# Kernel optimization log

Measured on AMD Instinct MI355X. Metric: run time of the kernel, lower is better.

## Reference

```python
import jax, jax.numpy as jnp
import numpy as np

EPS = 1e-6
WEACH = 10  # width chunk size


def layernorm2d(x, w, b):
    # channel-wise LN per (b,h,w): x [B,C,H,W]
    mu = x.mean(axis=1, keepdims=True)
    var = ((x - mu) ** 2).mean(axis=1, keepdims=True)
    y = (x - mu) / jnp.sqrt(var + EPS)
    return w[None, :, None, None] * y + b[None, :, None, None]


def conv1x1(x, w, b):
    # w [O,I], x [B,I,H,W]
    return jnp.einsum('oi,bihw->bohw', w, x) + b[None, :, None, None]


def dynamic_conv1x1(x, y, fc1w, fc1b, fc2w, fc2b, W, bias):
    # attention2d on y -> per-sample mixture over K expert 1x1 convs applied to x
    gap = y.mean(axis=(2, 3))                          # [B,C]
    a = jax.nn.relu(gap @ fc1w.T + fc1b)               # [B,K]
    a = a @ fc2w.T + fc2b                              # [B,K]
    att = jax.nn.softmax(a, axis=-1)                   # [B,K]
    Wagg = jnp.einsum('bk,koi->boi', att, W)           # [B,O,I]
    bagg = att @ bias                                  # [B,O]
    return jnp.einsum('boi,bihw->bohw', Wagg, x) + bagg[:, :, None, None]


def _chunk(t, nW):
    # [B,C,H,W] -> [B,C,H,nW,WEACH]
    B, C, H, W = t.shape
    return t.reshape(B, C, H, nW, WEACH)


def reference(x_l, x_r,
              norm_l_w, norm_l_b, norm_r_w, norm_r_b,
              lp1_w, lp1_b, rp1_w, rp1_b,
              lp2_w, lp2_b, rp2_w, rp2_b,
              beta, gamma,
              lf_fc1w, lf_fc1b, lf_fc2w, lf_fc2b, lf_W, lf_bias,
              rf_fc1w, rf_fc1b, rf_fc2w, rf_fc2b, rf_W, rf_bias):
    B, C, H, W = x_l.shape
    nW = W // WEACH
    scale = C ** (-0.5)

    # LayerNorm and 1x1 projections are pointwise -> compute on full tensor
    Ql = _chunk(conv1x1(layernorm2d(x_l, norm_l_w, norm_l_b), lp1_w, lp1_b), nW)
    Qr = _chunk(conv1x1(layernorm2d(x_r, norm_r_w, norm_r_b), rp1_w, rp1_b), nW)
    Vl = _chunk(conv1x1(x_l, lp2_w, lp2_b), nW)
    Vr = _chunk(conv1x1(x_r, rp2_w, rp2_b), nW)

    # block-diagonal attention within each width chunk, per height row
    attn = jnp.einsum('bchnu,bchnv->bhnuv', Ql, Qr) * scale   # [B,H,nW,10,10]
    A_r2l = jax.nn.softmax(attn, axis=-1)                     # softmax over v (right positions)
    A_l2r = jax.nn.softmax(attn, axis=-2)                     # softmax over u (left positions)
    F_r2l = jnp.einsum('bhnuv,bchnv->bchnu', A_r2l, Vr)       # [B,C,H,nW,10]
    F_l2r = jnp.einsum('bhnuv,bchnu->bchnv', A_l2r, Vl)

    F_r2l = F_r2l.reshape(B, C, H, W) * beta
    F_l2r = F_l2r.reshape(B, C, H, W) * gamma

    # dynamic per-batch 1x1 grouped conv, conditioned on the shortcut branch
    out_rl = dynamic_conv1x1(F_r2l, x_l, lf_fc1w, lf_fc1b, lf_fc2w, lf_fc2b, lf_W, lf_bias)
    out_lr = dynamic_conv1x1(F_l2r, x_r, rf_fc1w, rf_fc1b, rf_fc2w, rf_fc2b, rf_W, rf_bias)
    return (x_l + out_rl, x_r + out_lr)


def setup_inputs() -> dict:
    C, K = 64, 3
    B, H, W = 4, 180, 320
    key = jax.random.key(0)
    ks = jax.random.split(key, 24)
    n = lambda k, s, sc=0.05: jax.random.normal(k, s, dtype=jnp.float32) * sc
    return {
        'x_l': jax.random.normal(ks[0], (B, C, H, W), dtype=jnp.float32),
        'x_r': jax.random.normal(ks[1], (B, C, H, W), dtype=jnp.float32),
        'norm_l_w': jnp.ones((C,), jnp.float32), 'norm_l_b': jnp.zeros((C,), jnp.float32),
        'norm_r_w': jnp.ones((C,), jnp.float32), 'norm_r_b': jnp.zeros((C,), jnp.float32),
        'lp1_w': n(ks[2], (C, C)), 'lp1_b': jnp.zeros((C,), jnp.float32),
        'rp1_w': n(ks[3], (C, C)), 'rp1_b': jnp.zeros((C,), jnp.float32),
        'lp2_w': n(ks[4], (C, C)), 'lp2_b': jnp.zeros((C,), jnp.float32),
        'rp2_w': n(ks[5], (C, C)), 'rp2_b': jnp.zeros((C,), jnp.float32),
        'beta': n(ks[6], (1, C, 1, 1), 0.1), 'gamma': n(ks[7], (1, C, 1, 1), 0.1),
        'lf_fc1w': n(ks[8], (K, C)), 'lf_fc1b': jnp.zeros((K,), jnp.float32),
        'lf_fc2w': n(ks[9], (K, K)), 'lf_fc2b': jnp.zeros((K,), jnp.float32),
        'lf_W': n(ks[10], (K, C, C)), 'lf_bias': n(ks[11], (K, C), 0.01),
        'rf_fc1w': n(ks[12], (K, C)), 'rf_fc1b': jnp.zeros((K,), jnp.float32),
        'rf_fc2w': n(ks[13], (K, K)), 'rf_fc2b': jnp.zeros((K,), jnp.float32),
        'rf_W': n(ks[14], (K, C, C)), 'rf_bias': n(ks[15], (K, C), 0.01),
    }
```

## Files before the change

### kernel.cpp

```cpp
#include <hip/hip_runtime.h>

typedef unsigned int u32;

#define BB 4
#define HH 180
#define WWD 320
#define HW_ 57600
#define TENSOR_ 14745600
#define XM 84
#define QS 68

__device__ __align__(16) float g_gap[512];
__device__ __align__(16) float g_bagg[512];
__device__ __align__(16) float g_swn[128];
__device__ __align__(16) float g_sb[128];
__device__ __align__(16) float g_waggT[32768];
__device__ __align__(16) float g_w1fT[8192];
__device__ __align__(16) float g_p2T[8192];

__global__ __launch_bounds__(256) void gap_kernel(const float* __restrict__ xl,
                                                  const float* __restrict__ xr) {
    int job = blockIdx.x;
    int side = job >> 8;
    int bc = job & 255;
    const float4* p = (const float4*)((side ? xr : xl) + (size_t)bc * HW_);
    float s = 0.f;
    for (int i = threadIdx.x; i < 14400; i += 256) {
        float4 v = p[i];
        s += v.x + v.y + v.z + v.w;
    }
    #pragma unroll
    for (int off = 32; off > 0; off >>= 1) s += __shfl_down(s, off, 64);
    __shared__ float red[4];
    int lane = threadIdx.x & 63, wv = threadIdx.x >> 6;
    if (lane == 0) red[wv] = s;
    __syncthreads();
    if (threadIdx.x == 0)
        g_gap[job] = (red[0] + red[1] + red[2] + red[3]) * (1.f / 57600.f);
}

__global__ __launch_bounds__(256) void prep_kernel(
    const float* __restrict__ nlw, const float* __restrict__ nlb,
    const float* __restrict__ nrw, const float* __restrict__ nrb,
    const float* __restrict__ lp1w, const float* __restrict__ rp1w,
    const float* __restrict__ lp2w, const float* __restrict__ rp2w,
    const float* __restrict__ lf1w, const float* __restrict__ lf1b,
    const float* __restrict__ lf2w, const float* __restrict__ lf2b,
    const float* __restrict__ lfbias,
    const float* __restrict__ rf1w, const float* __restrict__ rf1b,
    const float* __restrict__ rf2w, const float* __restrict__ rf2b,
    const float* __restrict__ rfbias,
    const float* __restrict__ lfW, const float* __restrict__ rfW)
{
    __shared__ float att[2][4][3];
    int t = threadIdx.x;
    if (t < 8) {
        int side = t >> 2, b = t & 3;
        const float* f1w = side ? rf1w : lf1w;
        const float* f1b = side ? rf1b : lf1b;
        const float* f2w = side ? rf2w : lf2w;
        const float* f2bv = side ? rf2b : lf2b;
        const float* g = g_gap + side*256 + b*64;
        float a1[3];
        #pragma unroll
        for (int k = 0; k < 3; k++) {
            float s = f1b[k];
            for (int c = 0; c < 64; c++) s += g[c] * f1w[k*64 + c];
            a1[k] = fmaxf(s, 0.f);
        }
        float a2[3];
        #pragma unroll
        for (int j = 0; j < 3; j++) {
            float s = f2bv[j];
            #pragma unroll
            for (int k = 0; k < 3; k++) s += a1[k] * f2w[j*3 + k];
            a2[j] = s;
        }
        float m = fmaxf(fmaxf(a2[0], a2[1]), a2[2]);
        float e0 = __expf(a2[0]-m), e1 = __expf(a2[1]-m), e2 = __expf(a2[2]-m);
        float inv = 1.f / (e0 + e1 + e2);
        att[side][b][0] = e0*inv; att[side][b][1] = e1*inv; att[side][b][2] = e2*inv;
    }
    __syncthreads();

    if (blockIdx.x < 16) {
        int flat = blockIdx.x * 2048 + t * 8;
        int side = flat >> 14, bb = (flat >> 12) & 3, i = (flat >> 6) & 63, o0 = flat & 63;
        const float* Wp = side ? rfW : lfW;
        float a0 = att[side][bb][0], a1 = att[side][bb][1], a2 = att[side][bb][2];
        #pragma unroll
        for (int q = 0; q < 8; q++) {
            int o = o0 + q;
            g_waggT[flat+q] = a0*Wp[o*64+i] + a1*Wp[4096+o*64+i] + a2*Wp[8192+o*64+i];
        }
    } else {
        if (t < 128) {
            int side = t >> 6, o = t & 63;
            const float* w1 = side ? rp1w : lp1w;
            const float* w2 = side ? rp2w : lp2w;
            const float* nw = side ? nrw : nlw;
            const float* nb = side ? nrb : nlb;
            float s_wn = 0.f, s_b = 0.f;
            for (int i = 0; i < 64; i++) {
                float wf = w1[o*64 + i];
                float wp = wf * nw[i];
                g_w1fT[side*4096 + i*64 + o] = wp;
                g_p2T [side*4096 + i*64 + o] = w2[o*64 + i];
                s_wn += wp;
                s_b  += wf * nb[i];
            }
            g_swn[side*64 + o] = s_wn;
            g_sb[side*64 + o]  = s_b;
        }
        for (int idx = t; idx < 512; idx += 256) {
            int side = idx >> 8, r = idx & 255, b = r >> 6, o = r & 63;
            const float* bp = side ? rfbias : lfbias;
            g_bagg[idx] = att[side][b][0]*bp[o]
                        + att[side][b][1]*bp[64+o]
                        + att[side][b][2]*bp[128+o];
        }
    }
}

__global__ __launch_bounds__(256, 3) void main_kernel(
    const float* __restrict__ xl_g, const float* __restrict__ xr_g,
    const float* __restrict__ lp1b, const float* __restrict__ rp1b,
    const float* __restrict__ lp2b, const float* __restrict__ rp2b,
    const float* __restrict__ beta, const float* __restrict__ gamma,
    float* __restrict__ out)
{
    __shared__ __align__(16) float xi0[2688];
    __shared__ __align__(16) float xi1[2688];
    __shared__ __align__(16) float qf0[2720];
    __shared__ __align__(16) float qf1[2720];
    __shared__ float attn[4][10][10];
    __shared__ float Ar[4][10][10];
    __shared__ float Al[4][10][10];
    __shared__ float muA[40], rsA[40], muB[40], rsB[40];

    int t = threadIdx.x;
    int wv = t >> 6, lane = t & 63;
    int bid = blockIdx.x;
    int b  = bid / (HH*8);
    int r0 = bid % (HH*8);
    int h  = r0 / 8;
    int g  = r0 % 8;
    int w0 = g * 40;

    for (int idx = t; idx < 640; idx += 256) {
        int tensor = idx / 320;
        int r2 = idx - tensor*320;
        int m = r2 / 10, seg = r2 - m*10;
        const float* src = (tensor ? xr_g : xl_g)
                         + (((size_t)(b*64 + 2*m)*HH + h)*WWD + w0 + seg*4);
        float4 a = *(const float4*)(src);
        float4 c = *(const float4*)(src + HW_);
        float* dst = (tensor ? xi1 : xi0) + m*XM + seg*8;
        *(float4*)(dst)     = make_float4(a.x, c.x, a.y, c.y);
        *(float4*)(dst + 4) = make_float4(a.z, c.z, a.w, c.w);
    }
    __syncthreads();

    if (lane < 20) {
        int side = wv >> 1;
        int u = (wv & 1)*20 + lane;
        const float* xx = side ? xi1 : xi0;
        float s = 0.f, s2 = 0.f;
        for (int m = 0; m < 32; m++) {
            float v0 = xx[m*XM + u*2];
            float v1 = xx[m*XM + u*2 + 1];
            s += v0 + v1; s2 += v0*v0 + v1*v1;
        }
        float mu = s * (1.f/64.f);
        float var = fmaxf(s2 * (1.f/64.f) - mu*mu, 0.f);
        float rs = rsqrtf(var + 1e-6f);
        if (side) { muB[u] = mu; rsB[u] = rs; } else { muA[u] = mu; rsA[u] = rs; }
    }
    __syncthreads();

    int og = lane & 7, ug = lane >> 3;
    int ob = og * 8, ub = ug * 5;

    float acc[8][5];
    #pragma unroll
    for (int r = 0; r < 8; r++)
        #pragma unroll
        for (int j = 0; j < 5; j++) acc[r][j] = 0.f;

    {
        const float* wT; const float* xs;
        switch (wv) {
            case 0:  wT = g_w1fT;        xs = xi0; break;
            case 1:  wT = g_w1fT + 4096; xs = xi1; break;
            case 2:  wT = g_p2T;         xs = xi0; break;
            default: wT = g_p2T + 4096;  xs = xi1; break;
        }
        __builtin_amdgcn_s_setprio(1);
        for (int m = 0; m < 32; m++) {
            const float* wp = wT + m*128;
            float4 wa0 = *(const float4*)(wp + ob);
            float4 wa1 = *(const float4*)(wp + ob + 4);
            float4 wb0 = *(const float4*)(wp + 64 + ob);
            float4 wb1 = *(const float4*)(wp + 64 + ob + 4);
            float2 xv[5];
            const float* xrow = xs + m*XM + ub*2;
            #pragma unroll
            for (int j = 0; j < 5; j++) xv[j] = *(const float2*)(xrow + j*2);
            float wa[8] = {wa0.x,wa0.y,wa0.z,wa0.w, wa1.x,wa1.y,wa1.z,wa1.w};
            float wb[8] = {wb0.x,wb0.y,wb0.z,wb0.w, wb1.x,wb1.y,wb1.z,wb1.w};
            #pragma unroll
            for (int r = 0; r < 8; r++)
                #pragma unroll
                for (int j = 0; j < 5; j++) {
                    acc[r][j] = fmaf(wa[r], xv[j].x, acc[r][j]);
                    acc[r][j] = fmaf(wb[r], xv[j].y, acc[r][j]);
                }
        }
        __builtin_amdgcn_s_setprio(0);
    }

    if (wv < 2) {
        const float* mu  = wv ? muB : muA;
        const float* rs  = wv ? rsB : rsA;
        const float* p1b = wv ? rp1b : lp1b;
        float* qdst = wv ? qf1 : qf0;
        float swl[8], sbl[8];
        #pragma unroll
        for (int r = 0; r < 8; r++) {
            swl[r] = g_swn[wv*64 + ob + r];
            sbl[r] = g_sb[wv*64 + ob + r] + p1b[ob + r];
        }
        #pragma unroll
        for (int j = 0; j < 5; j++) {
            int u = ub + j;
            float rsv = rs[u], muv = mu[u];
            float e[8];
            #pragma unroll
            for (int r = 0; r < 8; r++)
                e[r] = rsv*(acc[r][j] - muv*swl[r]) + sbl[r];
            *(float4*)(qdst + u*QS + ob)     = make_float4(e[0],e[1],e[2],e[3]);
            *(float4*)(qdst + u*QS + ob + 4) = make_float4(e[4],e[5],e[6],e[7]);
        }
    } else {
        const float* p2b = (wv == 2) ? lp2b : rp2b;
        #pragma unroll
        for (int r = 0; r < 8; r++) {
            float bv = p2b[ob + r];
            #pragma unroll
            for (int j = 0; j < 5; j++) acc[r][j] += bv;
        }
    }
    __syncthreads();

    for (int p = lane; p < 100; p += 64) {
        int uu = p / 10, vv = p - (p/10)*10;
        const float4* ra = (const float4*)(qf0 + (wv*10 + uu)*QS);
        const float4* rb = (const float4*)(qf1 + (wv*10 + vv)*QS);
        float s = 0.f;
        #pragma unroll
        for (int cc = 0; cc < 16; cc++) {
            float4 a = ra[cc], q = rb[cc];
            s += a.x*q.x + a.y*q.y + a.z*q.z + a.w*q.w;
        }
        attn[wv][uu][vv] = s * 0.125f;
    }
    __syncthreads();

    if (t < 40) {
        int k = t / 10, uu = t - (t/10)*10;
        float m = attn[k][uu][0];
        #pragma unroll
        for (int v2 = 1; v2 < 10; v2++) m = fmaxf(m, attn[k][uu][v2]);
        float e[10]; float ssum = 0.f;
        #pragma unroll
        for (int v2 = 0; v2 < 10; v2++) { e[v2] = __expf(attn[k][uu][v2] - m); ssum += e[v2]; }
        float inv = 1.f / ssum;
        #pragma unroll
        for (int v2 = 0; v2 < 10; v2++) Ar[k][uu][v2] = e[v2]*inv;
    } else if (t >= 64 && t < 104) {
        int t2 = t - 64;
        int k = t2 / 10, vv = t2 - (t2/10)*10;
        float m = attn[k][0][vv];
        #pragma unroll
        for (int u2 = 1; u2 < 10; u2++) m = fmaxf(m, attn[k][u2][vv]);
        float e[10]; float ssum = 0.f;
        #pragma unroll
        for (int u2 = 0; u2 < 10; u2++) { e[u2] = __expf(attn[k][u2][vv] - m); ssum += e[u2]; }
        float inv = 1.f / ssum;
        #pragma unroll
        for (int u2 = 0; u2 < 10; u2++) Al[k][u2][vv] = e[u2]*inv;
    }
    __syncthreads();

    if (wv == 3) {
        int k = ug >> 1, half = ug & 1, vb = half*5;
        float sc[8];
        #pragma unroll
        for (int r = 0; r < 8; r++) sc[r] = beta[ob + r];
        #pragma unroll
        for (int j2 = 0; j2 < 5; j2++) {
            int u1 = vb + j2;
            int u2 = 5 - vb + j2;
            float a1[5], a2[5];
            #pragma unroll
            for (int j = 0; j < 5; j++) { a1[j] = Ar[k][u1][vb+j]; a2[j] = Ar[k][u2][vb+j]; }
            #pragma unroll
            for (int r = 0; r < 8; r++) {
                float sA = 0.f, sB = 0.f;
                #pragma unroll
                for (int j = 0; j < 5; j++) {
                    sA = fmaf(a1[j], acc[r][j], sA);
                    sB = fmaf(a2[j], acc[r][j], sB);
                }
                float recv = __shfl_xor(sB, 8, 64);
                int o = ob + r;
                qf0[(o>>1)*XM + (k*10 + u1)*2 + (o&1)] = (sA + recv) * sc[r];
            }
        }
    } else if (wv == 2) {
        int k = ug >> 1, half = ug & 1, vb = half*5;
        float sc[8];
        #pragma unroll
        for (int r = 0; r < 8; r++) sc[r] = gamma[ob + r];
        #pragma unroll
        for (int j2 = 0; j2 < 5; j2++) {
            int u1 = vb + j2;
            int u2 = 5 - vb + j2;
            float a1[5], a2[5];
            #pragma unroll
            for (int j = 0; j < 5; j++) { a1[j] = Al[k][vb+j][u1]; a2[j] = Al[k][vb+j][u2]; }
            #pragma unroll
            for (int r = 0; r < 8; r++) {
                float sA = 0.f, sB = 0.f;
                #pragma unroll
                for (int j = 0; j < 5; j++) {
                    sA = fmaf(a1[j], acc[r][j], sA);
                    sB = fmaf(a2[j], acc[r][j], sB);
                }
                float recv = __shfl_xor(sB, 8, 64);
                int o = ob + r;
                qf1[(o>>1)*XM + (k*10 + u1)*2 + (o&1)] = (sA + recv) * sc[r];
            }
        }
    }
    __syncthreads();

    {
        int side = wv >> 1;
        int oh   = wv & 1;
        int ob4  = oh*32 + og*4;
        const float* Fb   = side ? qf1 : qf0;
        const float* xres = side ? xi1 : xi0;
        const float* wrow = g_waggT + (size_t)(side*4 + b)*4096;
        float acc5[4][5];
        #pragma unroll
        for (int r = 0; r < 4; r++)
            #pragma unroll
            for (int j = 0; j < 5; j++) acc5[r][j] = 0.f;
        __builtin_amdgcn_s_setprio(1);
        for (int m = 0; m < 32; m++) {
            const float* wp = wrow + m*128;
            float4 wa4 = *(const float4*)(wp + ob4);
            float4 wb4 = *(const float4*)(wp + 64 + ob4);
            float2 xv[5];
            const float* frow = Fb + m*XM + ub*2;
            #pragma unroll
            for (int j = 0; j < 5; j++) xv[j] = *(const float2*)(frow + j*2);
            float wa[4] = {wa4.x,wa4.y,wa4.z,wa4.w};
            float wb[4] = {wb4.x,wb4.y,wb4.z,wb4.w};
            #pragma unroll
            for (int r = 0; r < 4; r++)
                #pragma unroll
                for (int j = 0; j < 5; j++) {
                    acc5[r][j] = fmaf(wa[r], xv[j].x, acc5[r][j]);
                    acc5[r][j] = fmaf(wb[r], xv[j].y, acc5[r][j]);
                }
        }
        __builtin_amdgcn_s_setprio(0);
        #pragma unroll
        for (int r = 0; r < 4; r++) {
            int o = ob4 + r;
            float bg = g_bagg[side*256 + b*64 + o];
            float* op = out + (size_t)side*TENSOR_ + (((size_t)(b*64+o)*HH + h)*WWD + w0 + ub);
            #pragma unroll
            for (int j = 0; j < 5; j++)
                op[j] = acc5[r][j] + bg + xres[(o>>1)*XM + (ub+j)*2 + (o&1)];
        }
    }
}

extern "C" void kernel_launch(void* const* d_in, const int* in_sizes, int n_in,
                              void* d_out, int out_size, void* d_ws, size_t ws_size,
                              hipStream_t stream) {
    (void)in_sizes; (void)n_in; (void)out_size; (void)d_ws; (void)ws_size;
    const float* x_l = (const float*)d_in[0];
    const float* x_r = (const float*)d_in[1];

    gap_kernel<<<512, 256, 0, stream>>>(x_l, x_r);
    prep_kernel<<<17, 256, 0, stream>>>(
        (const float*)d_in[2],  (const float*)d_in[3],
        (const float*)d_in[4],  (const float*)d_in[5],
        (const float*)d_in[6],  (const float*)d_in[8],
        (const float*)d_in[10], (const float*)d_in[12],
        (const float*)d_in[16], (const float*)d_in[17],
        (const float*)d_in[18], (const float*)d_in[19], (const float*)d_in[21],
        (const float*)d_in[22], (const float*)d_in[23],
        (const float*)d_in[24], (const float*)d_in[25], (const float*)d_in[27],
        (const float*)d_in[20], (const float*)d_in[26]);
    main_kernel<<<BB*HH*8, 256, 0, stream>>>(x_l, x_r,
        (const float*)d_in[7],  (const float*)d_in[9],
        (const float*)d_in[11], (const float*)d_in[13],
        (const float*)d_in[14], (const float*)d_in[15],
        (float*)d_out);
}
```

Measured before the change: 482.1 us.

## Convert LDS tiles and weights to packed fp16 and use fdot2 for projections

Weights, input tiles and intermediate Q/F features are now stored as packed half2 in shared memory and global scratch. The 1x1 projection, attention-score and output conv loops use v_dot2 (fdot2) with fp32 accumulation instead of pairs of fp32 FMAs. Shared memory per block is roughly halved and occupancy hints rise from 3 to 5 blocks. The residual is reloaded from global fp32 instead of the LDS copy. Precision drops to fp16 inputs, which risks accuracy for LayerNorm statistics and the residual path.

Measured after the change: 436.5 us. 9.5% less time.

```diff
diff --git a/kernel.cpp b/kernel.cpp
--- a/kernel.cpp
+++ b/kernel.cpp
@@ -1,22 +1,25 @@
 #include <hip/hip_runtime.h>
 
 typedef unsigned int u32;
+typedef __fp16 h2 __attribute__((ext_vector_type(2)));
 
 #define BB 4
 #define HH 180
 #define WWD 320
 #define HW_ 57600
 #define TENSOR_ 14745600
-#define XM 84
-#define QS 68
+#define XST 44
+#define QST 36
+
+union U4 { float4 f; h2 h[4]; };
 
 __device__ __align__(16) float g_gap[512];
 __device__ __align__(16) float g_bagg[512];
 __device__ __align__(16) float g_swn[128];
 __device__ __align__(16) float g_sb[128];
-__device__ __align__(16) float g_waggT[32768];
-__device__ __align__(16) float g_w1fT[8192];
-__device__ __align__(16) float g_p2T[8192];
+__device__ __align__(16) h2 g_w1fTh[4096];
+__device__ __align__(16) h2 g_p2Th[4096];
+__device__ __align__(16) h2 g_waggTh[16384];
 
 __global__ __launch_bounds__(256) void gap_kernel(const float* __restrict__ xl,
                                                   const float* __restrict__ xr) {
@@ -84,14 +87,16 @@
     __syncthreads();
 
     if (blockIdx.x < 16) {
-        int flat = blockIdx.x * 2048 + t * 8;
-        int side = flat >> 14, bb = (flat >> 12) & 3, i = (flat >> 6) & 63, o0 = flat & 63;
+        int flat2 = blockIdx.x * 1024 + t * 4;
+        int side = flat2 >> 13, bb = (flat2 >> 11) & 3, m = (flat2 >> 6) & 31, o0 = flat2 & 63;
         const float* Wp = side ? rfW : lfW;
         float a0 = att[side][bb][0], a1 = att[side][bb][1], a2 = att[side][bb][2];
         #pragma unroll
-        for (int q = 0; q < 8; q++) {
+        for (int q = 0; q < 4; q++) {
             int o = o0 + q;
-            g_waggT[flat+q] = a0*Wp[o*64+i] + a1*Wp[4096+o*64+i] + a2*Wp[8192+o*64+i];
+            float wi0 = a0*Wp[o*64+2*m]   + a1*Wp[4096+o*64+2*m]   + a2*Wp[8192+o*64+2*m];
+            float wi1 = a0*Wp[o*64+2*m+1] + a1*Wp[4096+o*64+2*m+1] + a2*Wp[8192+o*64+2*m+1];
+            g_waggTh[((side*4+bb)*32 + m)*64 + o] = __builtin_amdgcn_cvt_pkrtz(wi0, wi1);
         }
     } else {
         if (t < 128) {
@@ -101,13 +106,15 @@
             const float* nw = side ? nrw : nlw;
             const float* nb = side ? nrb : nlb;
             float s_wn = 0.f, s_b = 0.f;
-            for (int i = 0; i < 64; i++) {
-                float wf = w1[o*64 + i];
-                float wp = wf * nw[i];
-                g_w1fT[side*4096 + i*64 + o] = wp;
-                g_p2T [side*4096 + i*64 + o] = w2[o*64 + i];
-                s_wn += wp;
-                s_b  += wf * nb[i];
+            for (int m = 0; m < 32; m++) {
+                float wf0 = w1[o*64 + 2*m],   wf1 = w1[o*64 + 2*m+1];
+                float wp0 = wf0 * nw[2*m],    wp1 = wf1 * nw[2*m+1];
+                h2 hw = __builtin_amdgcn_cvt_pkrtz(wp0, wp1);
+                g_w1fTh[side*2048 + m*64 + o] = hw;
+                g_p2Th [side*2048 + m*64 + o] =
+                    __builtin_amdgcn_cvt_pkrtz(w2[o*64+2*m], w2[o*64+2*m+1]);
+                s_wn += (float)hw.x + (float)hw.y;
+                s_b  += wf0*nb[2*m] + wf1*nb[2*m+1];
             }
             g_swn[side*64 + o] = s_wn;
             g_sb[side*64 + o]  = s_b;
@@ -122,17 +129,17 @@
     }
 }
 
-__global__ __launch_bounds__(256, 3) void main_kernel(
+__global__ __launch_bounds__(256, 5) void main_kernel(
     const float* __restrict__ xl_g, const float* __restrict__ xr_g,
     const float* __restrict__ lp1b, const float* __restrict__ rp1b,
     const float* __restrict__ lp2b, const float* __restrict__ rp2b,
     const float* __restrict__ beta, const float* __restrict__ gamma,
     float* __restrict__ out)
 {
-    __shared__ __align__(16) float xi0[2688];
-    __shared__ __align__(16) float xi1[2688];
-    __shared__ __align__(16) float qf0[2720];
-    __shared__ __align__(16) float qf1[2720];
+    __shared__ __align__(16) h2 xi0[1408];
+    __shared__ __align__(16) h2 xi1[1408];
+    __shared__ __align__(16) h2 qf0[1440];
+    __shared__ __align__(16) h2 qf1[1440];
     __shared__ float attn[4][10][10];
     __shared__ float Ar[4][10][10];
     __shared__ float Al[4][10][10];
@@ -155,22 +162,31 @@
                          + (((size_t)(b*64 + 2*m)*HH + h)*WWD + w0 + seg*4);
         float4 a = *(const float4*)(src);
         float4 c = *(const float4*)(src + HW_);
-        float* dst = (tensor ? xi1 : xi0) + m*XM + seg*8;
-        *(float4*)(dst)     = make_float4(a.x, c.x, a.y, c.y);
-        *(float4*)(dst + 4) = make_float4(a.z, c.z, a.w, c.w);
+        U4 u;
+        u.h[0] = __builtin_amdgcn_cvt_pkrtz(a.x, c.x);
+        u.h[1] = __builtin_amdgcn_cvt_pkrtz(a.y, c.y);
+        u.h[2] = __builtin_amdgcn_cvt_pkrtz(a.z, c.z);
+        u.h[3] = __builtin_amdgcn_cvt_pkrtz(a.w, c.w);
+        h2* dst = (tensor ? xi1 : xi0) + m*XST + seg*4;
+        *(float4*)dst = u.f;
     }
     __syncthreads();
 
     if (lane < 20) {
         int side = wv >> 1;
         int u = (wv & 1)*20 + lane;
-        const float* xx = side ? xi1 : xi0;
-        float s = 0.f, s2 = 0.f;
-        for (int m = 0; m < 32; m++) {
-            float v0 = xx[m*XM + u*2];
-            float v1 = xx[m*XM + u*2 + 1];
-            s += v0 + v1; s2 += v0*v0 + v1*v1;
-        }
+        const h2* xx = side ? xi1 : xi0;
+        h2 one2; one2.x = (__fp16)1.f; one2.y = (__fp16)1.f;
+        float s_0 = 0.f, s_1 = 0.f, q_0 = 0.f, q_1 = 0.f;
+        for (int m = 0; m < 32; m += 2) {
+            h2 v0 = xx[m*XST + u];
+            h2 v1 = xx[(m+1)*XST + u];
+            s_0 = __builtin_amdgcn_fdot2(v0, one2, s_0, false);
+            q_0 = __builtin_amdgcn_fdot2(v0, v0,   q_0, false);
+            s_1 = __builtin_amdgcn_fdot2(v1, one2, s_1, false);
+            q_1 = __builtin_amdgcn_fdot2(v1, v1,   q_1, false);
+        }
+        float s = s_0 + s_1, s2 = q_0 + q_1;
         float mu = s * (1.f/64.f);
         float var = fmaxf(s2 * (1.f/64.f) - mu*mu, 0.f);
         float rs = rsqrtf(var + 1e-6f);
@@ -188,33 +204,30 @@
         for (int j = 0; j < 5; j++) acc[r][j] = 0.f;
 
     {
-        const float* wT; const float* xs;
+        const h2* wT; const h2* xs;
         switch (wv) {
-            case 0:  wT = g_w1fT;        xs = xi0; break;
-            case 1:  wT = g_w1fT + 4096; xs = xi1; break;
-            case 2:  wT = g_p2T;         xs = xi0; break;
-            default: wT = g_p2T + 4096;  xs = xi1; break;
+            case 0:  wT = g_w1fTh;        xs = xi0; break;
+            case 1:  wT = g_w1fTh + 2048; xs = xi1; break;
+            case 2:  wT = g_p2Th;         xs = xi0; break;
+            default: wT = g_p2Th + 2048;  xs = xi1; break;
         }
         __builtin_amdgcn_s_setprio(1);
         for (int m = 0; m < 32; m++) {
-            const float* wp = wT + m*128;
-            float4 wa0 = *(const float4*)(wp + ob);
-            float4 wa1 = *(const float4*)(wp + ob + 4);
-            float4 wb0 = *(const float4*)(wp + 64 + ob);
-            float4 wb1 = *(const float4*)(wp + 64 + ob + 4);
-            float2 xv[5];
-            const float* xrow = xs + m*XM + ub*2;
-            #pragma unroll
-            for (int j = 0; j < 5; j++) xv[j] = *(const float2*)(xrow + j*2);
-            float wa[8] = {wa0.x,wa0.y,wa0.z,wa0.w, wa1.x,wa1.y,wa1.z,wa1.w};
-            float wb[8] = {wb0.x,wb0.y,wb0.z,wb0.w, wb1.x,wb1.y,wb1.z,wb1.w};
+            const h2* wp = wT + m*64 + ob;
+            U4 w0u, w1u;
+            w0u.f = *(const float4*)(wp);
+            w1u.f = *(const float4*)(wp + 4);
+            h2 xv[5];
+            const h2* xrow = xs + m*XST + ub;
+            #pragma unroll
+            for (int j = 0; j < 5; j++) xv[j] = xrow[j];
+            h2 wa[8] = {w0u.h[0],w0u.h[1],w0u.h[2],w0u.h[3],
+                        w1u.h[0],w1u.h[1],w1u.h[2],w1u.h[3]};
             #pragma unroll
             for (int r = 0; r < 8; r++)
                 #pragma unroll
-                for (int j = 0; j < 5; j++) {
-                    acc[r][j] = fmaf(wa[r], xv[j].x, acc[r][j]);
-                    acc[r][j] = fmaf(wb[r], xv[j].y, acc[r][j]);
-                }
+                for (int j = 0; j < 5; j++)
+                    acc[r][j] = __builtin_amdgcn_fdot2(wa[r], xv[j], acc[r][j], false);
         }
         __builtin_amdgcn_s_setprio(0);
     }
@@ -223,7 +236,7 @@
         const float* mu  = wv ? muB : muA;
         const float* rs  = wv ? rsB : rsA;
         const float* p1b = wv ? rp1b : lp1b;
-        float* qdst = wv ? qf1 : qf0;
+        h2* qdst = wv ? qf1 : qf0;
         float swl[8], sbl[8];
         #pragma unroll
         for (int r = 0; r < 8; r++) {
@@ -238,8 +251,12 @@
             #pragma unroll
             for (int r = 0; r < 8; r++)
                 e[r] = rsv*(acc[r][j] - muv*swl[r]) + sbl[r];
-            *(float4*)(qdst + u*QS + ob)     = make_float4(e[0],e[1],e[2],e[3]);
-            *(float4*)(qdst + u*QS + ob + 4) = make_float4(e[4],e[5],e[6],e[7]);
+            U4 q;
+            q.h[0] = __builtin_amdgcn_cvt_pkrtz(e[0], e[1]);
+            q.h[1] = __builtin_amdgcn_cvt_pkrtz(e[2], e[3]);
+            q.h[2] = __builtin_amdgcn_cvt_pkrtz(e[4], e[5]);
+            q.h[3] = __builtin_amdgcn_cvt_pkrtz(e[6], e[7]);
+            *(float4*)(qdst + u*QST + og*4) = q.f;
         }
     } else {
         const float* p2b = (wv == 2) ? lp2b : rp2b;
@@ -254,15 +271,17 @@
 
     for (int p = lane; p < 100; p += 64) {
         int uu = p / 10, vv = p - (p/10)*10;
-        const float4* ra = (const float4*)(qf0 + (wv*10 + uu)*QS);
-        const float4* rb = (const float4*)(qf1 + (wv*10 + vv)*QS);
-        float s = 0.f;
-        #pragma unroll
-        for (int cc = 0; cc < 16; cc++) {
-            float4 a = ra[cc], q = rb[cc];
-            s += a.x*q.x + a.y*q.y + a.z*q.z + a.w*q.w;
-        }
-        attn[wv][uu][vv] = s * 0.125f;
+        const h2* ra = qf0 + (wv*10 + uu)*QST;
+        const h2* rb = qf1 + (wv*10 + vv)*QST;
+        float sa = 0.f, sb = 0.f, sc = 0.f, sd = 0.f;
+        #pragma unroll
+        for (int c2 = 0; c2 < 32; c2 += 4) {
+            sa = __builtin_amdgcn_fdot2(ra[c2],   rb[c2],   sa, false);
+            sb = __builtin_amdgcn_fdot2(ra[c2+1], rb[c2+1], sb, false);
+            sc = __builtin_amdgcn_fdot2(ra[c2+2], rb[c2+2], sc, false);
+            sd = __builtin_amdgcn_fdot2(ra[c2+3], rb[c2+3], sd, false);
+        }
+        attn[wv][uu][vv] = ((sa+sb)+(sc+sd)) * 0.125f;
     }
     __syncthreads();
 
@@ -304,6 +323,7 @@
             float a1[5], a2[5];
             #pragma unroll
             for (int j = 0; j < 5; j++) { a1[j] = Ar[k][u1][vb+j]; a2[j] = Ar[k][u2][vb+j]; }
+            float fv[8];
             #pragma unroll
             for (int r = 0; r < 8; r++) {
                 float sA = 0.f, sB = 0.f;
@@ -313,9 +333,12 @@
                     sB = fmaf(a2[j], acc[r][j], sB);
                 }
                 float recv = __shfl_xor(sB, 8, 64);
-                int o = ob + r;
-                qf0[(o>>1)*XM + (k*10 + u1)*2 + (o&1)] = (sA + recv) * sc[r];
+                fv[r] = (sA + recv) * sc[r];
             }
+            #pragma unroll
+            for (int rr = 0; rr < 4; rr++)
+                qf0[(og*4+rr)*XST + k*10 + u1] =
+                    __builtin_amdgcn_cvt_pkrtz(fv[2*rr], fv[2*rr+1]);
         }
     } else if (wv == 2) {
         int k = ug >> 1, half = ug & 1, vb = half*5;
@@ -329,6 +352,7 @@
             float a1[5], a2[5];
             #pragma unroll
             for (int j = 0; j < 5; j++) { a1[j] = Al[k][vb+j][u1]; a2[j] = Al[k][vb+j][u2]; }
+            float fv[8];
             #pragma unroll
             for (int r = 0; r < 8; r++) {
                 float sA = 0.f, sB = 0.f;
@@ -338,9 +362,12 @@
                     sB = fmaf(a2[j], acc[r][j], sB);
                 }
                 float recv = __shfl_xor(sB, 8, 64);
-                int o = ob + r;
-                qf1[(o>>1)*XM + (k*10 + u1)*2 + (o&1)] = (sA + recv) * sc[r];
+                fv[r] = (sA + recv) * sc[r];
             }
+            #pragma unroll
+            for (int rr = 0; rr < 4; rr++)
+                qf1[(og*4+rr)*XST + k*10 + u1] =
+                    __builtin_amdgcn_cvt_pkrtz(fv[2*rr], fv[2*rr+1]);
         }
     }
     __syncthreads();
@@ -349,9 +376,18 @@
         int side = wv >> 1;
         int oh   = wv & 1;
         int ob4  = oh*32 + og*4;
-        const float* Fb   = side ? qf1 : qf0;
-        const float* xres = side ? xi1 : xi0;
-        const float* wrow = g_waggT + (size_t)(side*4 + b)*4096;
+        const h2* Fb = side ? qf1 : qf0;
+        const h2* wrow = g_waggTh + (size_t)(side*4 + b)*2048;
+        const float* xsrc = side ? xr_g : xl_g;
+
+        float res[4][5];
+        #pragma unroll
+        for (int r = 0; r < 4; r++) {
+            const float* rp = xsrc + (size_t)(b*64 + ob4 + r)*HW_ + (size_t)h*WWD + w0 + ub;
+            #pragma unroll
+            for (int j = 0; j < 5; j++) res[r][j] = rp[j];
+        }
+
         float acc5[4][5];
         #pragma unroll
         for (int r = 0; r < 4; r++)
@@ -359,22 +395,17 @@
             for (int j = 0; j < 5; j++) acc5[r][j] = 0.f;
         __builtin_amdgcn_s_setprio(1);
         for (int m = 0; m < 32; m++) {
-            const float* wp = wrow + m*128;
-            float4 wa4 = *(const float4*)(wp + ob4);
-            float4 wb4 = *(const float4*)(wp + 64 + ob4);
-            float2 xv[5];
-            const float* frow = Fb + m*XM + ub*2;
-            #pragma unroll
-            for (int j = 0; j < 5; j++) xv[j] = *(const float2*)(frow + j*2);
-            float wa[4] = {wa4.x,wa4.y,wa4.z,wa4.w};
-            float wb[4] = {wb4.x,wb4.y,wb4.z,wb4.w};
+            U4 wu;
+            wu.f = *(const float4*)(wrow + m*64 + ob4);
+            h2 xv[5];
+            const h2* frow = Fb + m*XST + ub;
+            #pragma unroll
+            for (int j = 0; j < 5; j++) xv[j] = frow[j];
             #pragma unroll
             for (int r = 0; r < 4; r++)
                 #pragma unroll
-                for (int j = 0; j < 5; j++) {
-                    acc5[r][j] = fmaf(wa[r], xv[j].x, acc5[r][j]);
-                    acc5[r][j] = fmaf(wb[r], xv[j].y, acc5[r][j]);
-                }
+                for (int j = 0; j < 5; j++)
+                    acc5[r][j] = __builtin_amdgcn_fdot2(wu.h[r], xv[j], acc5[r][j], false);
         }
         __builtin_amdgcn_s_setprio(0);
         #pragma unroll
@@ -384,7 +415,7 @@
             float* op = out + (size_t)side*TENSOR_ + (((size_t)(b*64+o)*HH + h)*WWD + w0 + ub);
             #pragma unroll
             for (int j = 0; j < 5; j++)
-                op[j] = acc5[r][j] + bg + xres[(o>>1)*XM + (ub+j)*2 + (o&1)];
+                op[j] = acc5[r][j] + bg + res[r][j];
         }
     }
 }
```

## Move main kernel matmuls to fp16 MFMA with half-precision LDS tiles

Applied to the files above, without the earlier changes.

Replaces the scalar fp32 FMA loops for the 1x1 projections, attention scores, attention-weighted value mixing and dynamic conv with 16x16x32 fp16 MFMA instructions. Weights are pre-packed to fp16 pairs in the prep kernel, biases are folded there, and activations are staged in LDS as fp16, which shrinks shared memory and allows the occupancy hint to rise from 3 to 4 blocks. The residual is re-read from global memory in fp32 instead of being kept in LDS. Using fp16 inputs adds rounding error relative to the fp32 reference and pads tiles from 40 to 48 pixels.

After: 388.6 us. 19.4% less time.

```diff
diff --git a/kernel.cpp b/kernel.cpp
--- a/kernel.cpp
+++ b/kernel.cpp
@@ -1,22 +1,26 @@
 #include <hip/hip_runtime.h>
 
 typedef unsigned int u32;
+typedef __fp16 h2  __attribute__((ext_vector_type(2)));
+typedef __fp16 v8h __attribute__((ext_vector_type(8)));
+typedef float  f32x4 __attribute__((ext_vector_type(4)));
 
 #define BB 4
 #define HH 180
 #define WWD 320
 #define HW_ 57600
 #define TENSOR_ 14745600
-#define XM 84
-#define QS 68
+
+union U4 { float4 f; v8h h8; h2 h[4]; };
 
 __device__ __align__(16) float g_gap[512];
 __device__ __align__(16) float g_bagg[512];
 __device__ __align__(16) float g_swn[128];
 __device__ __align__(16) float g_sb[128];
-__device__ __align__(16) float g_waggT[32768];
-__device__ __align__(16) float g_w1fT[8192];
-__device__ __align__(16) float g_p2T[8192];
+__device__ __align__(16) float g_vb[128];
+__device__ __align__(16) h2 g_w1fH[4096];
+__device__ __align__(16) h2 g_p2H[4096];
+__device__ __align__(16) h2 g_waggH[16384];
 
 __global__ __launch_bounds__(256) void gap_kernel(const float* __restrict__ xl,
                                                   const float* __restrict__ xr) {
@@ -44,6 +48,8 @@
     const float* __restrict__ nrw, const float* __restrict__ nrb,
     const float* __restrict__ lp1w, const float* __restrict__ rp1w,
     const float* __restrict__ lp2w, const float* __restrict__ rp2w,
+    const float* __restrict__ lp1b, const float* __restrict__ rp1b,
+    const float* __restrict__ lp2b, const float* __restrict__ rp2b,
     const float* __restrict__ lf1w, const float* __restrict__ lf1b,
     const float* __restrict__ lf2w, const float* __restrict__ lf2b,
     const float* __restrict__ lfbias,
@@ -84,14 +90,18 @@
     __syncthreads();
 
     if (blockIdx.x < 16) {
-        int flat = blockIdx.x * 2048 + t * 8;
-        int side = flat >> 14, bb = (flat >> 12) & 3, i = (flat >> 6) & 63, o0 = flat & 63;
+        int flat = blockIdx.x * 256 + t;
+        int row = flat >> 3, seg = flat & 7;
+        int side = row >> 8, bb = (row >> 6) & 3, o = row & 63;
         const float* Wp = side ? rfW : lfW;
         float a0 = att[side][bb][0], a1 = att[side][bb][1], a2 = att[side][bb][2];
         #pragma unroll
-        for (int q = 0; q < 8; q++) {
-            int o = o0 + q;
-            g_waggT[flat+q] = a0*Wp[o*64+i] + a1*Wp[4096+o*64+i] + a2*Wp[8192+o*64+i];
+        for (int e = 0; e < 4; e++) {
+            int m = seg*4 + e;
+            int i0 = 2*m;
+            float wi0 = a0*Wp[o*64+i0]   + a1*Wp[4096+o*64+i0]   + a2*Wp[8192+o*64+i0];
+            float wi1 = a0*Wp[o*64+i0+1] + a1*Wp[4096+o*64+i0+1] + a2*Wp[8192+o*64+i0+1];
+            g_waggH[row*32 + m] = __builtin_amdgcn_cvt_pkrtz(wi0, wi1);
         }
     } else {
         if (t < 128) {
@@ -100,17 +110,21 @@
             const float* w2 = side ? rp2w : lp2w;
             const float* nw = side ? nrw : nlw;
             const float* nb = side ? nrb : nlb;
+            const float* b1 = side ? rp1b : lp1b;
+            const float* b2 = side ? rp2b : lp2b;
             float s_wn = 0.f, s_b = 0.f;
-            for (int i = 0; i < 64; i++) {
-                float wf = w1[o*64 + i];
-                float wp = wf * nw[i];
-                g_w1fT[side*4096 + i*64 + o] = wp;
-                g_p2T [side*4096 + i*64 + o] = w2[o*64 + i];
-                s_wn += wp;
-                s_b  += wf * nb[i];
+            for (int m = 0; m < 32; m++) {
+                float wf0 = w1[o*64 + 2*m],   wf1 = w1[o*64 + 2*m+1];
+                h2 hw = __builtin_amdgcn_cvt_pkrtz(wf0 * nw[2*m], wf1 * nw[2*m+1]);
+                g_w1fH[(side*64 + o)*32 + m] = hw;
+                g_p2H [(side*64 + o)*32 + m] =
+                    __builtin_amdgcn_cvt_pkrtz(w2[o*64+2*m], w2[o*64+2*m+1]);
+                s_wn += (float)hw.x + (float)hw.y;
+                s_b  += wf0*nb[2*m] + wf1*nb[2*m+1];
             }
             g_swn[side*64 + o] = s_wn;
-            g_sb[side*64 + o]  = s_b;
+            g_sb[side*64 + o]  = s_b + b1[o];
+            g_vb[side*64 + o]  = b2[o];
         }
         for (int idx = t; idx < 512; idx += 256) {
             int side = idx >> 8, r = idx & 255, b = r >> 6, o = r & 63;
@@ -122,24 +136,20 @@
     }
 }
 
-__global__ __launch_bounds__(256, 3) void main_kernel(
+__global__ __launch_bounds__(256, 4) void main_kernel(
     const float* __restrict__ xl_g, const float* __restrict__ xr_g,
-    const float* __restrict__ lp1b, const float* __restrict__ rp1b,
-    const float* __restrict__ lp2b, const float* __restrict__ rp2b,
     const float* __restrict__ beta, const float* __restrict__ gamma,
     float* __restrict__ out)
 {
-    __shared__ __align__(16) float xi0[2688];
-    __shared__ __align__(16) float xi1[2688];
-    __shared__ __align__(16) float qf0[2720];
-    __shared__ __align__(16) float qf1[2720];
+    __shared__ __align__(16) h2 xA[2][48][36];
+    __shared__ __align__(16) __fp16 qA[2][48][72];
     __shared__ float attn[4][10][10];
-    __shared__ float Ar[4][10][10];
-    __shared__ float Al[4][10][10];
-    __shared__ float muA[40], rsA[40], muB[40], rsB[40];
+    __shared__ __align__(16) __fp16 AH[2][4][16][32];
+    __shared__ float muS[2][48], rsS[2][48];
 
     int t = threadIdx.x;
     int wv = t >> 6, lane = t & 63;
+    int g16 = lane >> 4, i16 = lane & 15;
     int bid = blockIdx.x;
     int b  = bid / (HH*8);
     int r0 = bid % (HH*8);
@@ -147,122 +157,133 @@
     int g  = r0 % 8;
     int w0 = g * 40;
 
-    for (int idx = t; idx < 640; idx += 256) {
-        int tensor = idx / 320;
-        int r2 = idx - tensor*320;
-        int m = r2 / 10, seg = r2 - m*10;
-        const float* src = (tensor ? xr_g : xl_g)
-                         + (((size_t)(b*64 + 2*m)*HH + h)*WWD + w0 + seg*4);
-        float4 a = *(const float4*)(src);
-        float4 c = *(const float4*)(src + HW_);
-        float* dst = (tensor ? xi1 : xi0) + m*XM + seg*8;
-        *(float4*)(dst)     = make_float4(a.x, c.x, a.y, c.y);
-        *(float4*)(dst + 4) = make_float4(a.z, c.z, a.w, c.w);
-    }
-    __syncthreads();
-
-    if (lane < 20) {
-        int side = wv >> 1;
-        int u = (wv & 1)*20 + lane;
-        const float* xx = side ? xi1 : xi0;
+    f32x4 z4; z4[0]=0.f; z4[1]=0.f; z4[2]=0.f; z4[3]=0.f;
+
+    for (int idx = t; idx < 1216; idx += 256) {
+        if (idx < 640) {
+            int tensor = idx / 320;
+            int r2 = idx - tensor*320;
+            int m = r2 / 10, seg = r2 - m*10;
+            const float* src = (tensor ? xr_g : xl_g)
+                             + (((size_t)(b*64 + 2*m)*HH + h)*WWD + w0 + seg*4);
+            float4 a = *(const float4*)(src);
+            float4 c = *(const float4*)(src + HW_);
+            xA[tensor][seg*4+0][m] = __builtin_amdgcn_cvt_pkrtz(a.x, c.x);
+            xA[tensor][seg*4+1][m] = __builtin_amdgcn_cvt_pkrtz(a.y, c.y);
+            xA[tensor][seg*4+2][m] = __builtin_amdgcn_cvt_pkrtz(a.z, c.z);
+            xA[tensor][seg*4+3][m] = __builtin_amdgcn_cvt_pkrtz(a.w, c.w);
+        } else {
+            int z = idx - 640;
+            int side = z / 288, rr = z - side*288;
+            int row = 40 + rr/36, col = rr - (rr/36)*36;
+            h2 hz; hz.x = (__fp16)0.f; hz.y = (__fp16)0.f;
+            xA[side][row][col] = hz;
+        }
+    }
+    __syncthreads();
+
+    if (t < 96) {
+        int side = t / 48, u = t - side*48;
+        const h2* row = &xA[side][u][0];
+        h2 one2; one2.x = (__fp16)1.f; one2.y = (__fp16)1.f;
         float s = 0.f, s2 = 0.f;
-        for (int m = 0; m < 32; m++) {
-            float v0 = xx[m*XM + u*2];
-            float v1 = xx[m*XM + u*2 + 1];
-            s += v0 + v1; s2 += v0*v0 + v1*v1;
+        #pragma unroll
+        for (int q = 0; q < 8; q++) {
+            U4 v; v.f = *(const float4*)(row + q*4);
+            #pragma unroll
+            for (int e = 0; e < 4; e++) {
+                s  = __builtin_amdgcn_fdot2(v.h[e], one2,   s,  false);
+                s2 = __builtin_amdgcn_fdot2(v.h[e], v.h[e], s2, false);
+            }
         }
         float mu = s * (1.f/64.f);
         float var = fmaxf(s2 * (1.f/64.f) - mu*mu, 0.f);
-        float rs = rsqrtf(var + 1e-6f);
-        if (side) { muB[u] = mu; rsB[u] = rs; } else { muA[u] = mu; rsA[u] = rs; }
-    }
-    __syncthreads();
-
-    int og = lane & 7, ug = lane >> 3;
-    int ob = og * 8, ub = ug * 5;
-
-    float acc[8][5];
-    #pragma unroll
-    for (int r = 0; r < 8; r++)
-        #pragma unroll
-        for (int j = 0; j < 5; j++) acc[r][j] = 0.f;
+        muS[side][u] = mu;
+        rsS[side][u] = rsqrtf(var + 1e-6f);
+    }
+    __syncthreads();
 
     {
-        const float* wT; const float* xs;
-        switch (wv) {
-            case 0:  wT = g_w1fT;        xs = xi0; break;
-            case 1:  wT = g_w1fT + 4096; xs = xi1; break;
-            case 2:  wT = g_p2T;         xs = xi0; break;
-            default: wT = g_p2T + 4096;  xs = xi1; break;
-        }
+        int side = wv & 1;
+        const h2* wTab = ((wv < 2) ? g_w1fH : g_p2H) + side*2048;
+        f32x4 acc[4][3];
+        #pragma unroll
+        for (int mt = 0; mt < 4; mt++)
+            #pragma unroll
+            for (int nt = 0; nt < 3; nt++) acc[mt][nt] = z4;
+
         __builtin_amdgcn_s_setprio(1);
-        for (int m = 0; m < 32; m++) {
-            const float* wp = wT + m*128;
-            float4 wa0 = *(const float4*)(wp + ob);
-            float4 wa1 = *(const float4*)(wp + ob + 4);
-            float4 wb0 = *(const float4*)(wp + 64 + ob);
-            float4 wb1 = *(const float4*)(wp + 64 + ob + 4);
-            float2 xv[5];
-            const float* xrow = xs + m*XM + ub*2;
-            #pragma unroll
-            for (int j = 0; j < 5; j++) xv[j] = *(const float2*)(xrow + j*2);
-            float wa[8] = {wa0.x,wa0.y,wa0.z,wa0.w, wa1.x,wa1.y,wa1.z,wa1.w};
-            float wb[8] = {wb0.x,wb0.y,wb0.z,wb0.w, wb1.x,wb1.y,wb1.z,wb1.w};
-            #pragma unroll
-            for (int r = 0; r < 8; r++)
+        #pragma unroll
+        for (int kt = 0; kt < 2; kt++) {
+            U4 bf[3];
+            #pragma unroll
+            for (int nt = 0; nt < 3; nt++)
+                bf[nt].f = *(const float4*)(&xA[side][nt*16 + i16][kt*16 + g16*4]);
+            #pragma unroll
+            for (int mt = 0; mt < 4; mt++) {
+                U4 af; af.f = *(const float4*)(wTab + (mt*16 + i16)*32 + kt*16 + g16*4);
                 #pragma unroll
-                for (int j = 0; j < 5; j++) {
-                    acc[r][j] = fmaf(wa[r], xv[j].x, acc[r][j]);
-                    acc[r][j] = fmaf(wb[r], xv[j].y, acc[r][j]);
+                for (int nt = 0; nt < 3; nt++)
+                    acc[mt][nt] = __builtin_amdgcn_mfma_f32_16x16x32_f16(
+                        af.h8, bf[nt].h8, acc[mt][nt], 0, 0, 0);
+            }
+        }
+        __builtin_amdgcn_s_setprio(0);
+        __syncthreads();
+
+        if (wv < 2) {
+            #pragma unroll
+            for (int nt = 0; nt < 3; nt++) {
+                int u = nt*16 + i16;
+                float mu = muS[side][u], rs = rsS[side][u];
+                #pragma unroll
+                for (int mt = 0; mt < 4; mt++) {
+                    float4 swl = *(const float4*)&g_swn[side*64 + mt*16 + g16*4];
+                    float4 sbl = *(const float4*)&g_sb [side*64 + mt*16 + g16*4];
+                    f32x4 a = acc[mt][nt];
+                    float e0 = rs*(a[0] - mu*swl.x) + sbl.x;
+                    float e1 = rs*(a[1] - mu*swl.y) + sbl.y;
+                    float e2 = rs*(a[2] - mu*swl.z) + sbl.z;
+                    float e3 = rs*(a[3] - mu*swl.w) + sbl.w;
+                    h2* dst = (h2*)&qA[side][u][mt*16 + g16*4];
+                    dst[0] = __builtin_amdgcn_cvt_pkrtz(e0, e1);
+                    dst[1] = __builtin_amdgcn_cvt_pkrtz(e2, e3);
                 }
-        }
-        __builtin_amdgcn_s_setprio(0);
-    }
-
-    if (wv < 2) {
-        const float* mu  = wv ? muB : muA;
-        const float* rs  = wv ? rsB : rsA;
-        const float* p1b = wv ? rp1b : lp1b;
-        float* qdst = wv ? qf1 : qf0;
-        float swl[8], sbl[8];
-        #pragma unroll
-        for (int r = 0; r < 8; r++) {
-            swl[r] = g_swn[wv*64 + ob + r];
-            sbl[r] = g_sb[wv*64 + ob + r] + p1b[ob + r];
-        }
-        #pragma unroll
-        for (int j = 0; j < 5; j++) {
-            int u = ub + j;
-            float rsv = rs[u], muv = mu[u];
-            float e[8];
-            #pragma unroll
-            for (int r = 0; r < 8; r++)
-                e[r] = rsv*(acc[r][j] - muv*swl[r]) + sbl[r];
-            *(float4*)(qdst + u*QS + ob)     = make_float4(e[0],e[1],e[2],e[3]);
-            *(float4*)(qdst + u*QS + ob + 4) = make_float4(e[4],e[5],e[6],e[7]);
-        }
-    } else {
-        const float* p2b = (wv == 2) ? lp2b : rp2b;
-        #pragma unroll
-        for (int r = 0; r < 8; r++) {
-            float bv = p2b[ob + r];
-            #pragma unroll
-            for (int j = 0; j < 5; j++) acc[r][j] += bv;
-        }
-    }
-    __syncthreads();
-
-    for (int p = lane; p < 100; p += 64) {
-        int uu = p / 10, vv = p - (p/10)*10;
-        const float4* ra = (const float4*)(qf0 + (wv*10 + uu)*QS);
-        const float4* rb = (const float4*)(qf1 + (wv*10 + vv)*QS);
-        float s = 0.f;
-        #pragma unroll
-        for (int cc = 0; cc < 16; cc++) {
-            float4 a = ra[cc], q = rb[cc];
-            s += a.x*q.x + a.y*q.y + a.z*q.z + a.w*q.w;
-        }
-        attn[wv][uu][vv] = s * 0.125f;
+            }
+        } else {
+            __fp16* vTp = (__fp16*)xA;
+            #pragma unroll
+            for (int nt = 0; nt < 3; nt++) {
+                int px = nt*16 + i16;
+                #pragma unroll
+                for (int mt = 0; mt < 4; mt++) {
+                    float4 vb = *(const float4*)&g_vb[side*64 + mt*16 + g16*4];
+                    f32x4 a = acc[mt][nt];
+                    h2* dst = (h2*)&vTp[((size_t)side*48 + px)*72 + mt*16 + g16*4];
+                    dst[0] = __builtin_amdgcn_cvt_pkrtz(a[0]+vb.x, a[1]+vb.y);
+                    dst[1] = __builtin_amdgcn_cvt_pkrtz(a[2]+vb.z, a[3]+vb.w);
+                }
+            }
+        }
+    }
+    __syncthreads();
+
+    {
+        const __fp16* ra = &qA[0][wv*10 + i16][0];
+        const __fp16* rb = &qA[1][wv*10 + i16][0];
+        f32x4 s = z4;
+        #pragma unroll
+        for (int kt = 0; kt < 2; kt++) {
+            U4 af, bf;
+            af.f = *(const float4*)(ra + kt*32 + g16*8);
+            bf.f = *(const float4*)(rb + kt*32 + g16*8);
+            s = __builtin_amdgcn_mfma_f32_16x16x32_f16(af.h8, bf.h8, s, 0, 0, 0);
+        }
+        #pragma unroll
+        for (int reg = 0; reg < 4; reg++) {
+            int r = g16*4 + reg;
+            if (r < 10 && i16 < 10) attn[wv][r][i16] = s[reg] * 0.125f;
+        }
     }
     __syncthreads();
 
@@ -275,8 +296,17 @@
         #pragma unroll
         for (int v2 = 0; v2 < 10; v2++) { e[v2] = __expf(attn[k][uu][v2] - m); ssum += e[v2]; }
         float inv = 1.f / ssum;
-        #pragma unroll
-        for (int v2 = 0; v2 < 10; v2++) Ar[k][uu][v2] = e[v2]*inv;
+        h2 hz; hz.x = (__fp16)0.f; hz.y = (__fp16)0.f;
+        U4 r0_, r1_;
+        r0_.h[0] = __builtin_amdgcn_cvt_pkrtz(e[0]*inv, e[1]*inv);
+        r0_.h[1] = __builtin_amdgcn_cvt_pkrtz(e[2]*inv, e[3]*inv);
+        r0_.h[2] = __builtin_amdgcn_cvt_pkrtz(e[4]*inv, e[5]*inv);
+        r0_.h[3] = __builtin_amdgcn_cvt_pkrtz(e[6]*inv, e[7]*inv);
+        r1_.h[0] = __builtin_amdgcn_cvt_pkrtz(e[8]*inv, e[9]*inv);
+        r1_.h[1] = hz; r1_.h[2] = hz; r1_.h[3] = hz;
+        float4 zf = make_float4(0.f,0.f,0.f,0.f);
+        float4* dst = (float4*)&AH[0][k][uu][0];
+        dst[0] = r0_.f; dst[1] = r1_.f; dst[2] = zf; dst[3] = zf;
     } else if (t >= 64 && t < 104) {
         int t2 = t - 64;
         int k = t2 / 10, vv = t2 - (t2/10)*10;
@@ -287,104 +317,108 @@
         #pragma unroll
         for (int u2 = 0; u2 < 10; u2++) { e[u2] = __expf(attn[k][u2][vv] - m); ssum += e[u2]; }
         float inv = 1.f / ssum;
-        #pragma unroll
-        for (int u2 = 0; u2 < 10; u2++) Al[k][u2][vv] = e[u2]*inv;
-    }
-    __syncthreads();
-
-    if (wv == 3) {
-        int k = ug >> 1, half = ug & 1, vb = half*5;
-        float sc[8];
-        #pragma unroll
-        for (int r = 0; r < 8; r++) sc[r] = beta[ob + r];
-        #pragma unroll
-        for (int j2 = 0; j2 < 5; j2++) {
-            int u1 = vb + j2;
-            int u2 = 5 - vb + j2;
-            float a1[5], a2[5];
-            #pragma unroll
-            for (int j = 0; j < 5; j++) { a1[j] = Ar[k][u1][vb+j]; a2[j] = Ar[k][u2][vb+j]; }
-            #pragma unroll
-            for (int r = 0; r < 8; r++) {
-                float sA = 0.f, sB = 0.f;
+        h2 hz; hz.x = (__fp16)0.f; hz.y = (__fp16)0.f;
+        U4 r0_, r1_;
+        r0_.h[0] = __builtin_amdgcn_cvt_pkrtz(e[0]*inv, e[1]*inv);
+        r0_.h[1] = __builtin_amdgcn_cvt_pkrtz(e[2]*inv, e[3]*inv);
+        r0_.h[2] = __builtin_amdgcn_cvt_pkrtz(e[4]*inv, e[5]*inv);
+        r0_.h[3] = __builtin_amdgcn_cvt_pkrtz(e[6]*inv, e[7]*inv);
+        r1_.h[0] = __builtin_amdgcn_cvt_pkrtz(e[8]*inv, e[9]*inv);
+        r1_.h[1] = hz; r1_.h[2] = hz; r1_.h[3] = hz;
+        float4 zf = make_float4(0.f,0.f,0.f,0.f);
+        float4* dst = (float4*)&AH[1][k][vv][0];
+        dst[0] = r0_.f; dst[1] = r1_.f; dst[2] = zf; dst[3] = zf;
+    }
+    __syncthreads();
+
+    int side5 = wv >> 1, mth = wv & 1;
+    const float* xsrc = side5 ? xr_g : xl_g;
+    float res[2][3][4];
+    #pragma unroll
+    for (int m2 = 0; m2 < 2; m2++)
+        #pragma unroll
+        for (int nt = 0; nt < 3; nt++) {
+            int px = nt*16 + i16;
+            #pragma unroll
+            for (int reg = 0; reg < 4; reg++) {
+                int o = mth*32 + m2*16 + g16*4 + reg;
+                res[m2][nt][reg] = (px < 40)
+                    ? xsrc[(size_t)(b*64+o)*HW_ + (size_t)h*WWD + w0 + px] : 0.f;
+            }
+        }
+
+    {
+        int dir = wv >> 1, mth4 = wv & 1, vside = dir ^ 1;
+        const float* scp = dir ? gamma : beta;
+        const __fp16* vTp = (const __fp16*)xA;
+        #pragma unroll
+        for (int ch = 0; ch < 4; ch++) {
+            #pragma unroll
+            for (int m2 = 0; m2 < 2; m2++) {
+                int mt = mth4*2 + m2;
+                U4 af;
                 #pragma unroll
-                for (int j = 0; j < 5; j++) {
-                    sA = fmaf(a1[j], acc[r][j], sA);
-                    sB = fmaf(a2[j], acc[r][j], sB);
+                for (int j = 0; j < 8; j++) {
+                    int vv = ch*10 + g16*8 + j;
+                    vv = vv > 47 ? 47 : vv;
+                    af.h[j>>1][j&1] = vTp[((size_t)vside*48 + vv)*72 + mt*16 + i16];
                 }
-                float recv = __shfl_xor(sB, 8, 64);
-                int o = ob + r;
-                qf0[(o>>1)*XM + (k*10 + u1)*2 + (o&1)] = (sA + recv) * sc[r];
-            }
-        }
-    } else if (wv == 2) {
-        int k = ug >> 1, half = ug & 1, vb = half*5;
-        float sc[8];
-        #pragma unroll
-        for (int r = 0; r < 8; r++) sc[r] = gamma[ob + r];
-        #pragma unroll
-        for (int j2 = 0; j2 < 5; j2++) {
-            int u1 = vb + j2;
-            int u2 = 5 - vb + j2;
-            float a1[5], a2[5];
-            #pragma unroll
-            for (int j = 0; j < 5; j++) { a1[j] = Al[k][vb+j][u1]; a2[j] = Al[k][vb+j][u2]; }
-            #pragma unroll
-            for (int r = 0; r < 8; r++) {
-                float sA = 0.f, sB = 0.f;
+                U4 bf; bf.f = *(const float4*)&AH[dir][ch][i16][g16*8];
+                f32x4 d = __builtin_amdgcn_mfma_f32_16x16x32_f16(af.h8, bf.h8, z4, 0, 0, 0);
+                if (i16 < 10) {
+                    int px = ch*10 + i16;
+                    float4 sc = *(const float4*)&scp[mt*16 + g16*4];
+                    h2* dst = (h2*)&qA[dir][px][mt*16 + g16*4];
+                    dst[0] = __builtin_amdgcn_cvt_pkrtz(d[0]*sc.x, d[1]*sc.y);
+                    dst[1] = __builtin_amdgcn_cvt_pkrtz(d[2]*sc.z, d[3]*sc.w);
+                }
+            }
+        }
+    }
+    __syncthreads();
+
+    {
+        const h2* wag = g_waggH + (size_t)((side5*4 + b)*64 + mth*32)*32;
+        f32x4 acc[2][3];
+        #pragma unroll
+        for (int m2 = 0; m2 < 2; m2++)
+            #pragma unroll
+            for (int nt = 0; nt < 3; nt++) acc[m2][nt] = z4;
+
+        __builtin_amdgcn_s_setprio(1);
+        #pragma unroll
+        for (int kt = 0; kt < 2; kt++) {
+            U4 bf[3];
+            #pragma unroll
+            for (int nt = 0; nt < 3; nt++)
+                bf[nt].f = *(const float4*)(&qA[side5][nt*16 + i16][kt*32 + g16*8]);
+            #pragma unroll
+            for (int m2 = 0; m2 < 2; m2++) {
+                U4 af; af.f = *(const float4*)(wag + (m2*16 + i16)*32 + kt*16 + g16*4);
                 #pragma unroll
-                for (int j = 0; j < 5; j++) {
-                    sA = fmaf(a1[j], acc[r][j], sA);
-                    sB = fmaf(a2[j], acc[r][j], sB);
+                for (int nt = 0; nt < 3; nt++)
+                    acc[m2][nt] = __builtin_amdgcn_mfma_f32_16x16x32_f16(
+                        af.h8, bf[nt].h8, acc[m2][nt], 0, 0, 0);
+            }
+        }
+        __builtin_amdgcn_s_setprio(0);
+
+        #pragma unroll
+        for (int m2 = 0; m2 < 2; m2++) {
+            float4 bg = *(const float4*)&g_bagg[side5*256 + b*64 + mth*32 + m2*16 + g16*4];
+            float bga[4] = {bg.x, bg.y, bg.z, bg.w};
+            #pragma unroll
+            for (int nt = 0; nt < 3; nt++) {
+                int px = nt*16 + i16;
+                if (px < 40) {
+                    #pragma unroll
+                    for (int reg = 0; reg < 4; reg++) {
+                        int o = mth*32 + m2*16 + g16*4 + reg;
+                        out[(size_t)side5*TENSOR_ + (size_t)(b*64+o)*HW_ + (size_t)h*WWD + w0 + px]
+                            = acc[m2][nt][reg] + bga[reg] + res[m2][nt][reg];
+                    }
                 }
-                float recv = __shfl_xor(sB, 8, 64);
-                int o = ob + r;
-                qf1[(o>>1)*XM + (k*10 + u1)*2 + (o&1)] = (sA + recv) * sc[r];
-            }
-        }
-    }
-    __syncthreads();
-
-    {
-        int side = wv >> 1;
-        int oh   = wv & 1;
-        int ob4  = oh*32 + og*4;
-        const float* Fb   = side ? qf1 : qf0;
-        const float* xres = side ? xi1 : xi0;
-        const float* wrow = g_waggT + (size_t)(side*4 + b)*4096;
-        float acc5[4][5];
-        #pragma unroll
-        for (int r = 0; r < 4; r++)
-            #pragma unroll
-            for (int j = 0; j < 5; j++) acc5[r][j] = 0.f;
-        __builtin_amdgcn_s_setprio(1);
-        for (int m = 0; m < 32; m++) {
-            const float* wp = wrow + m*128;
-            float4 wa4 = *(const float4*)(wp + ob4);
-            float4 wb4 = *(const float4*)(wp + 64 + ob4);
-            float2 xv[5];
-            const float* frow = Fb + m*XM + ub*2;
-            #pragma unroll
-            for (int j = 0; j < 5; j++) xv[j] = *(const float2*)(frow + j*2);
-            float wa[4] = {wa4.x,wa4.y,wa4.z,wa4.w};
-            float wb[4] = {wb4.x,wb4.y,wb4.z,wb4.w};
-            #pragma unroll
-            for (int r = 0; r < 4; r++)
-                #pragma unroll
-                for (int j = 0; j < 5; j++) {
-                    acc5[r][j] = fmaf(wa[r], xv[j].x, acc5[r][j]);
-                    acc5[r][j] = fmaf(wb[r], xv[j].y, acc5[r][j]);
-                }
-        }
-        __builtin_amdgcn_s_setprio(0);
-        #pragma unroll
-        for (int r = 0; r < 4; r++) {
-            int o = ob4 + r;
-            float bg = g_bagg[side*256 + b*64 + o];
-            float* op = out + (size_t)side*TENSOR_ + (((size_t)(b*64+o)*HH + h)*WWD + w0 + ub);
-            #pragma unroll
-            for (int j = 0; j < 5; j++)
-                op[j] = acc5[r][j] + bg + xres[(o>>1)*XM + (ub+j)*2 + (o&1)];
+            }
         }
     }
 }
@@ -402,14 +436,14 @@
         (const float*)d_in[4],  (const float*)d_in[5],
         (const float*)d_in[6],  (const float*)d_in[8],
         (const float*)d_in[10], (const float*)d_in[12],
+        (const float*)d_in[7],  (const float*)d_in[9],
+        (const float*)d_in[11], (const float*)d_in[13],
         (const float*)d_in[16], (const float*)d_in[17],
         (const float*)d_in[18], (const float*)d_in[19], (const float*)d_in[21],
         (const float*)d_in[22], (const float*)d_in[23],
         (const float*)d_in[24], (const float*)d_in[25], (const float*)d_in[27],
         (const float*)d_in[20], (const float*)d_in[26]);
     main_kernel<<<BB*HH*8, 256, 0, stream>>>(x_l, x_r,
-        (const float*)d_in[7],  (const float*)d_in[9],
-        (const float*)d_in[11], (const float*)d_in[13],
         (const float*)d_in[14], (const float*)d_in[15],
         (float*)d_out);
 }
```
